# Kernel optimization log

Measured on AMD Instinct MI355X. Metric: run time of the kernel, lower is better.

## Reference

```python
import jax, jax.numpy as jnp
import numpy as np

HIDDEN = 1024
N_HEAD = 16
HEAD_DIM = HIDDEN // N_HEAD


def setup_inputs() -> dict:
    key = jax.random.key(0)
    k1, k2, k3 = jax.random.split(key, 3)
    B, S = 4, 2048
    x = jax.random.normal(k1, (B, S, HIDDEN), dtype=jnp.float32)
    # nn.Linear(hidden, 3*hidden, bias=False): weight [3*hidden, hidden]
    w_qkv = jax.random.normal(k2, (3 * HIDDEN, HIDDEN), dtype=jnp.float32) * (HIDDEN ** -0.5)
    w_out = jax.random.normal(k3, (HIDDEN, HIDDEN), dtype=jnp.float32) * (HIDDEN ** -0.5)
    return {"x": x, "w_qkv": w_qkv, "w_out": w_out}


def _rope(q, k):
    # q, k: [B, H, S, D]
    S, D = q.shape[-2], q.shape[-1]
    pos = jnp.arange(S, dtype=jnp.float32)[:, None]          # [S, 1]
    ids = jnp.arange(D // 2, dtype=jnp.float32)              # [D/2]
    theta = jnp.power(jnp.float32(10000.0), 2.0 * ids / D)   # [D/2]
    ang = pos / theta                                        # [S, D/2]
    # torch code: sin at even slots, cos at odd slots; then repeat_interleave(2)
    sin = jnp.repeat(jnp.sin(ang), 2, axis=-1)               # [S, D]
    cos = jnp.repeat(jnp.cos(ang), 2, axis=-1)               # [S, D]

    def rot(t):
        # stack([-t_odd, t_even], -1).reshape -> interleaved rotate-half
        t2 = jnp.stack([-t[..., 1::2], t[..., 0::2]], axis=-1).reshape(t.shape)
        return t * cos + t2 * sin

    return rot(q), rot(k)


def reference(x, w_qkv, w_out):
    B, S, _ = x.shape
    qkv = jnp.einsum('bsd,ed->bse', x, w_qkv)                # [B, S, 3*hidden]
    qkv = qkv.reshape(B, S, N_HEAD, 3 * HEAD_DIM).transpose(0, 2, 1, 3)  # [B,H,S,3D]
    q, k, v = jnp.split(qkv, 3, axis=-1)                     # each [B,H,S,D]
    q, k = _rope(q, k)
    # NOTE: original forward never applies self.scale, mask (eval), or dropout.
    scores = jnp.einsum('bhqd,bhkd->bhqk', q, k)             # [B,H,S,S]
    probs = jax.nn.softmax(scores, axis=-1)
    out = jnp.einsum('bhqk,bhkd->bhqd', probs, v)            # [B,H,S,D]
    out = out.transpose(0, 2, 1, 3).reshape(B, S, HIDDEN)
    return jnp.einsum('bsd,ed->bse', out, w_out)
```

## Files before the change

### kernel.cpp

```cpp
#include <hip/hip_runtime.h>
#include <stdint.h>
#include <math.h>

#define NHEAD 16
#define HDIM 64
#define BATCH 4
#define SEQ 2048
#define NROWS (BATCH*SEQ)
#define LOG2E 1.4426950408889634f

typedef _Float16 f16x8 __attribute__((ext_vector_type(8)));
typedef _Float16 f16x4 __attribute__((ext_vector_type(4)));
typedef __fp16 h16x2 __attribute__((ext_vector_type(2)));
typedef float f32x4 __attribute__((ext_vector_type(4)));
typedef float f32x16 __attribute__((ext_vector_type(16)));
typedef unsigned int u32x4 __attribute__((ext_vector_type(4)));

typedef const __attribute__((address_space(1))) unsigned int* gas_ptr;
typedef __attribute__((address_space(3))) unsigned int* las_ptr;

__device__ __forceinline__ void gload_lds16(const void* g, void* l) {
  __builtin_amdgcn_global_load_lds((gas_ptr)g, (las_ptr)l, 16, 0, 0);
}

__device__ __forceinline__ float exp2_fast(float x) {
  float r; asm("v_exp_f32 %0, %1" : "=v"(r) : "v"(x)); return r;
}

__device__ __forceinline__ float max3f(float a, float b, float c) {
  float r; asm("v_max3_f32 %0, %1, %2, %3" : "=v"(r) : "v"(a), "v"(b), "v"(c)); return r;
}

__device__ __forceinline__ unsigned pku(float a, float b) {
  h16x2 p = __builtin_amdgcn_cvt_pkrtz(a, b);
  return __builtin_bit_cast(unsigned, p);
}

__device__ __forceinline__ float xhalf_max(float a) {
  float b;
  asm volatile("v_mov_b32 %0, %1" : "=v"(b) : "v"(a));
  asm volatile("v_permlane32_swap_b32 %0, %1" : "+v"(a), "+v"(b));
  return fmaxf(a, b);
}

__global__ void prep_kernel(const float* __restrict__ x,
                            const float* __restrict__ wq,
                            const float* __restrict__ wo,
                            unsigned short* __restrict__ xb,
                            unsigned short* __restrict__ wqb,
                            unsigned short* __restrict__ wob,
                            float2* __restrict__ tab) {
  const int idx = blockIdx.x * blockDim.x + threadIdx.x;
  const int stride = gridDim.x * blockDim.x;
  const int NS = SEQ * 32;
  const int N1 = NROWS * 1024 / 4;
  const int N2 = 3072 * 1024 / 4;
  const int N3 = 1024 * 1024 / 4;

  if (idx < NS) {
    int s = idx >> 5, j = idx & 31;
    float theta = powf(10000.0f, (float)j / 32.0f);
    float ang = (float)s / theta;
    tab[idx] = make_float2(sinf(ang), cosf(ang));
  }
  for (int i = idx; i < N1 + N2 + N3; i += stride) {
    const float* src; unsigned short* dst; int k;
    if (i < N1)            { src = x;  dst = xb;  k = i; }
    else if (i < N1 + N2)  { src = wq; dst = wqb; k = i - N1; }
    else                   { src = wo; dst = wob; k = i - N1 - N2; }
    float4 v = ((const float4*)src)[k];
    f16x4 h;
    h[0] = (_Float16)v.x; h[1] = (_Float16)v.y;
    h[2] = (_Float16)v.z; h[3] = (_Float16)v.w;
    ((f16x4*)dst)[k] = h;
  }
}

__global__ __launch_bounds__(256)
void gemm_qkv_f16(const unsigned short* __restrict__ A,
                  const unsigned short* __restrict__ B,
                  const float2* __restrict__ tab,
                  unsigned short* __restrict__ Qh,
                  unsigned short* __restrict__ Kh,
                  unsigned short* __restrict__ Vt) {
  const int K = 1024, nk = K >> 6;
  __shared__ unsigned short sA[2][128 * 64];
  __shared__ unsigned short sB[2][128 * 64];
  const int tid = threadIdx.x;
  const int lane = tid & 63;
  const int wave = tid >> 6;
  const int wr = wave >> 1, wc = wave & 1;
  const long m0 = (long)blockIdx.x * 128;
  const long n0 = (long)blockIdx.y * 128;

  f32x16 acc[2][2] = {};

  auto stage = [&](int buf, int kt) {
    const long k0 = (long)kt * 64;
    const char* Ab = (const char*)A;
    const char* Bb = (const char*)B;
#pragma unroll
    for (int qd = 0; qd < 4; ++qd) {
      int o = qd * 4096 + tid * 16;
      int row = o >> 7;
      int colb = (((o >> 4) & 7) ^ (row & 7)) << 4;
      gload_lds16(Ab + ((m0 + row) * K + k0) * 2 + colb, (char*)&sA[buf][0] + o);
      gload_lds16(Bb + ((n0 + row) * K + k0) * 2 + colb, (char*)&sB[buf][0] + o);
    }
  };

  const int q32 = lane & 31, hi = lane >> 5, r7 = q32 & 7;
  int offA[2][4], offB[2][4];
#pragma unroll
  for (int t = 0; t < 2; ++t)
#pragma unroll
    for (int s = 0; s < 4; ++s) {
      offA[t][s] = (wr * 64 + t * 32 + q32) * 64 + (((s * 2 + hi) ^ r7) << 3);
      offB[t][s] = (wc * 64 + t * 32 + q32) * 64 + (((s * 2 + hi) ^ r7) << 3);
    }

  stage(0, 0);
  __syncthreads();
  int cur = 0;

  for (int kt = 0; kt < nk; ++kt) {
    if (kt + 1 < nk) stage(cur ^ 1, kt + 1);
#pragma unroll
    for (int s = 0; s < 4; ++s) {
      f16x8 a0 = *(const f16x8*)&sA[cur][offA[0][s]];
      f16x8 a1 = *(const f16x8*)&sA[cur][offA[1][s]];
      f16x8 b0 = *(const f16x8*)&sB[cur][offB[0][s]];
      f16x8 b1 = *(const f16x8*)&sB[cur][offB[1][s]];
      acc[0][0] = __builtin_amdgcn_mfma_f32_32x32x16_f16(a0, b0, acc[0][0], 0, 0, 0);
      acc[0][1] = __builtin_amdgcn_mfma_f32_32x32x16_f16(a0, b1, acc[0][1], 0, 0, 0);
      acc[1][0] = __builtin_amdgcn_mfma_f32_32x32x16_f16(a1, b0, acc[1][0], 0, 0, 0);
      acc[1][1] = __builtin_amdgcn_mfma_f32_32x32x16_f16(a1, b1, acc[1][1], 0, 0, 0);
    }
    __syncthreads();
    cur ^= 1;
  }

  const int rb0 = (int)m0 + wr * 64;
  const int bidx = rb0 >> 11;
  const int s0 = rb0 & 2047;
#pragma unroll
  for (int tn = 0; tn < 2; ++tn) {
    const int cbase = (int)n0 + wc * 64 + tn * 32;
    const int hh = cbase / 192;
    const int offc = cbase - hh * 192;
    const int part = offc >> 6;
    const int d = (offc & 63) + q32;
    const long bh_ = (long)(bidx * 16 + hh);
    if (part < 2) {
      _Float16* dst = (_Float16*)(part == 0 ? Qh : Kh) + bh_ * SEQ * 64 + d;
      const float qs = (part == 0) ? LOG2E : 1.0f;
      const float2* tp = tab + (d >> 1);
      const int sgn = q32 & 1;
#pragma unroll
      for (int tm = 0; tm < 2; ++tm)
#pragma unroll
        for (int rg = 0; rg < 16; ++rg) {
          int s = s0 + tm * 32 + (rg & 3) + 8 * (rg >> 2) + 4 * hi;
          float v = acc[tm][tn][rg];
          float p = __shfl_xor(v, 1, 64);
          float2 sc = tp[(long)s * 32];
          float rot = sgn ? (v * sc.y + p * sc.x) : (v * sc.y - p * sc.x);
          dst[(long)s * 64] = (_Float16)(rot * qs);
        }
    } else {
      _Float16* dst = (_Float16*)Vt + (bh_ * 64 + d) * SEQ;
#pragma unroll
      for (int tm = 0; tm < 2; ++tm)
#pragma unroll
        for (int rg = 0; rg < 16; ++rg) {
          int s = s0 + tm * 32 + (rg & 3) + 8 * (rg >> 2) + 4 * hi;
          dst[s] = (_Float16)acc[tm][tn][rg];
        }
    }
  }
}

__global__ __launch_bounds__(512, 4)
void attn_kernel(const unsigned short* __restrict__ Qh,
                 const unsigned short* __restrict__ Kh,
                 const unsigned short* __restrict__ Vt,
                 unsigned short* __restrict__ AOut) {
  __shared__ unsigned short sK[4][64 * 64];
  __shared__ unsigned short sV[4][64 * 64];

  const int NT = SEQ / 64;
  const int tid = threadIdx.x;
  const int w = tid >> 6, lane = tid & 63;
  const int q32 = lane & 31, hi = lane >> 5;

  const int bid = blockIdx.x;
  const int xcd = bid & 7, rest = bid >> 3;
  const int bh = (rest >> 3) * 8 + xcd;
  const int qt = rest & 7;
  const int b = bh >> 4, h = bh & 15;
  const int q = qt * 256 + w * 32 + q32;

  f16x8 aq[4];
#pragma unroll
  for (int ds = 0; ds < 4; ++ds)
    aq[ds] = *(const f16x8*)&Qh[((long)bh * SEQ + q) * 64 + ds * 16 + hi * 8];

  f32x16 acc0 = {}, acc1 = {}, accl = {};
  float mrow = -INFINITY;

  const int r7 = q32 & 7;
  int off[2][4];
#pragma unroll
  for (int t = 0; t < 2; ++t)
#pragma unroll
    for (int s = 0; s < 4; ++s)
      off[t][s] = (t * 32 + q32) * 64 + (((s * 2 + hi) ^ r7) << 3);

  const int cr = tid >> 3, cp = tid & 7, cps = cp ^ (cr & 7);
  const long kSrc0 = ((long)bh * SEQ + cr) * 64 + cps * 8;
  const long vSrc0 = ((long)bh * 64 + cr) * SEQ + cps * 8;

  auto stage = [&](int buf, int kt) {
    gload_lds16(&Kh[kSrc0 + (long)kt * 4096], (char*)&sK[buf][0] + tid * 16);
    gload_lds16(&Vt[vSrc0 + (long)kt * 64],   (char*)&sV[buf][0] + tid * 16);
  };

  f16x8 vones;
#pragma unroll
  for (int j = 0; j < 8; ++j) vones[j] = (_Float16)1.0f;

#define MKPA(dst, S, R0) {                                        \
    unsigned A0 = pku(S[R0 + 0], S[R0 + 1]);                      \
    unsigned A1 = pku(S[R0 + 2], S[R0 + 3]);                      \
    unsigned B0 = pku(S[R0 + 4], S[R0 + 5]);                      \
    unsigned B1 = pku(S[R0 + 6], S[R0 + 7]);                      \
    asm("v_permlane32_swap_b32 %0, %1" : "+v"(A0), "+v"(B0));     \
    asm("v_permlane32_swap_b32 %0, %1" : "+v"(A1), "+v"(B1));     \
    u32x4 tt; tt[0] = A0; tt[1] = A1; tt[2] = B0; tt[3] = B1;     \
    dst = __builtin_bit_cast(f16x8, tt); }

  auto tile = [&](int t) {
    const unsigned short* Kb = &sK[t & 3][0];
    const unsigned short* Vb = &sV[t & 3][0];

    f32x16 s0v = {}, s1v = {};
    __builtin_amdgcn_s_setprio(1);
#pragma unroll
    for (int ds = 0; ds < 4; ++ds) {
      f16x8 k0 = *(const f16x8*)&Kb[off[0][ds]];
      f16x8 k1 = *(const f16x8*)&Kb[off[1][ds]];
      s0v = __builtin_amdgcn_mfma_f32_32x32x16_f16(k0, aq[ds], s0v, 0, 0, 0);
      s1v = __builtin_amdgcn_mfma_f32_32x32x16_f16(k1, aq[ds], s1v, 0, 0, 0);
    }
    __builtin_amdgcn_s_setprio(0);

    float t0 = max3f(s0v[0], s0v[1], s0v[2]);
    float t1 = max3f(s0v[3], s0v[4], s0v[5]);
    float t2 = max3f(s0v[6], s0v[7], s0v[8]);
    float t3 = max3f(s0v[9], s0v[10], s0v[11]);
    float t4 = max3f(s0v[12], s0v[13], s0v[14]);
    float t5 = max3f(s0v[15], s1v[0], s1v[1]);
    float t6 = max3f(s1v[2], s1v[3], s1v[4]);
    float t7 = max3f(s1v[5], s1v[6], s1v[7]);
    float t8 = max3f(s1v[8], s1v[9], s1v[10]);
    float t9 = max3f(s1v[11], s1v[12], s1v[13]);
    float t10 = fmaxf(s1v[14], s1v[15]);
    float u0 = max3f(t0, t1, t2);
    float u1 = max3f(t3, t4, t5);
    float u2 = max3f(t6, t7, t8);
    float u3 = fmaxf(t9, t10);
    float tmax = xhalf_max(fmaxf(max3f(u0, u1, u2), u3));

    if (__any(tmax > mrow + 8.0f)) {
      float mnew = fmaxf(mrow, tmax);
      float al = exp2_fast(mrow - mnew);
      mrow = mnew;
#pragma unroll
      for (int r = 0; r < 16; ++r) { acc0[r] *= al; acc1[r] *= al; accl[r] *= al; }
    }
    const float mr = mrow;

#pragma unroll
    for (int r = 0; r < 16; ++r) {
      s0v[r] = exp2_fast(s0v[r] - mr);
      s1v[r] = exp2_fast(s1v[r] - mr);
    }

    f16x8 pa[4];
    MKPA(pa[0], s0v, 0);
    MKPA(pa[1], s0v, 8);
    MKPA(pa[2], s1v, 0);
    MKPA(pa[3], s1v, 8);

    __builtin_amdgcn_s_setprio(1);
#pragma unroll
    for (int ks = 0; ks < 4; ++ks) {
      f16x8 v0 = *(const f16x8*)&Vb[off[0][ks]];
      f16x8 v1 = *(const f16x8*)&Vb[off[1][ks]];
      acc0 = __builtin_amdgcn_mfma_f32_32x32x16_f16(v0, pa[ks], acc0, 0, 0, 0);
      acc1 = __builtin_amdgcn_mfma_f32_32x32x16_f16(v1, pa[ks], acc1, 0, 0, 0);
      accl = __builtin_amdgcn_mfma_f32_32x32x16_f16(vones, pa[ks], accl, 0, 0, 0);
    }
    __builtin_amdgcn_s_setprio(0);
  };

  stage(0, 0); stage(1, 1);
  __syncthreads();

  for (int it = 0; it < NT / 2; ++it) {
    const int t0 = it * 2;
    if (it + 1 < NT / 2) { stage((t0 + 2) & 3, t0 + 2); stage((t0 + 3) & 3, t0 + 3); }
    tile(t0);
    tile(t0 + 1);
    __syncthreads();
  }

  float inv = 1.f / accl[0];
  const long obase = ((long)b * SEQ + q) * 1024 + h * 64;
#define EPI(ACCV, DT)                                              \
  {                                                                \
    _Pragma("unroll")                                              \
    for (int rg = 0; rg < 4; ++rg) {                               \
      f16x4 o;                                                     \
      _Pragma("unroll")                                            \
      for (int e = 0; e < 4; ++e)                                  \
        o[e] = (_Float16)(ACCV[rg * 4 + e] * inv);                 \
      *(f16x4*)&AOut[obase + DT * 32 + rg * 8 + hi * 4] = o;       \
    }                                                              \
  }
  EPI(acc0, 0);
  EPI(acc1, 1);
}

__global__ __launch_bounds__(256)
void gemm_out_f16(const unsigned short* __restrict__ A,
                  const unsigned short* __restrict__ B,
                  float* __restrict__ C, int M, int N, int K) {
  __shared__ unsigned short sA[2][128 * 64];
  __shared__ unsigned short sB[2][128 * 64];
  const int tid = threadIdx.x;
  const int lane = tid & 63;
  const int wave = tid >> 6;
  const int wr = wave >> 1, wc = wave & 1;
  const long m0 = (long)blockIdx.x * 128;
  const long n0 = (long)blockIdx.y * 128;

  f32x16 acc[2][2] = {};

  auto stage = [&](int buf, int kt) {
    const long k0 = (long)kt * 64;
    const char* Ab = (const char*)A;
    const char* Bb = (const char*)B;
#pragma unroll
    for (int qd = 0; qd < 4; ++qd) {
      int o = qd * 4096 + tid * 16;
      int row = o >> 7;
      int colb = (((o >> 4) & 7) ^ (row & 7)) << 4;
      gload_lds16(Ab + ((m0 + row) * K + k0) * 2 + colb, (char*)&sA[buf][0] + o);
      gload_lds16(Bb + ((n0 + row) * K + k0) * 2 + colb, (char*)&sB[buf][0] + o);
    }
  };

  const int q32 = lane & 31, hi = lane >> 5, r7 = q32 & 7;
  int offA[2][4], offB[2][4];
#pragma unroll
  for (int t = 0; t < 2; ++t)
#pragma unroll
    for (int s = 0; s < 4; ++s) {
      offA[t][s] = (wr * 64 + t * 32 + q32) * 64 + (((s * 2 + hi) ^ r7) << 3);
      offB[t][s] = (wc * 64 + t * 32 + q32) * 64 + (((s * 2 + hi) ^ r7) << 3);
    }

  const int nk = K >> 6;
  stage(0, 0);
  __syncthreads();
  int cur = 0;

  for (int kt = 0; kt < nk; ++kt) {
    if (kt + 1 < nk) stage(cur ^ 1, kt + 1);
#pragma unroll
    for (int s = 0; s < 4; ++s) {
      f16x8 a0 = *(const f16x8*)&sA[cur][offA[0][s]];
      f16x8 a1 = *(const f16x8*)&sA[cur][offA[1][s]];
      f16x8 b0 = *(const f16x8*)&sB[cur][offB[0][s]];
      f16x8 b1 = *(const f16x8*)&sB[cur][offB[1][s]];
      acc[0][0] = __builtin_amdgcn_mfma_f32_32x32x16_f16(a0, b0, acc[0][0], 0, 0, 0);
      acc[0][1] = __builtin_amdgcn_mfma_f32_32x32x16_f16(a0, b1, acc[0][1], 0, 0, 0);
      acc[1][0] = __builtin_amdgcn_mfma_f32_32x32x16_f16(a1, b0, acc[1][0], 0, 0, 0);
      acc[1][1] = __builtin_amdgcn_mfma_f32_32x32x16_f16(a1, b1, acc[1][1], 0, 0, 0);
    }
    __syncthreads();
    cur ^= 1;
  }

  const long rbase = m0 + wr * 64;
#pragma unroll
  for (int tn = 0; tn < 2; ++tn) {
    const long col = n0 + wc * 64 + tn * 32 + q32;
#pragma unroll
    for (int tm = 0; tm < 2; ++tm)
#pragma unroll
      for (int rg = 0; rg < 16; ++rg) {
        long row = rbase + tm * 32 + (rg & 3) + 8 * (rg >> 2) + 4 * hi;
        C[row * N + col] = acc[tm][tn][rg];
      }
  }
}

extern "C" void kernel_launch(void* const* d_in, const int* in_sizes, int n_in,
                              void* d_out, int out_size, void* d_ws, size_t ws_size,
                              hipStream_t stream) {
  const float* x     = (const float*)d_in[0];
  const float* w_qkv = (const float*)d_in[1];
  const float* w_out = (const float*)d_in[2];
  float* out = (float*)d_out;
  char* ws = (char*)d_ws;

  unsigned short* xb    = (unsigned short*)(ws + 0);
  unsigned short* attnb = xb;
  unsigned short* wqkvb = (unsigned short*)(ws + 16777216);
  unsigned short* woutb = (unsigned short*)(ws + 23068672);
  unsigned short* Qh    = (unsigned short*)(ws + 25165824);
  unsigned short* Kh    = (unsigned short*)(ws + 41943040);
  unsigned short* Vt    = (unsigned short*)(ws + 58720256);
  float2*         tab   = (float2*)(ws + 75497472);

  prep_kernel<<<2048, 256, 0, stream>>>(x, w_qkv, w_out, xb, wqkvb, woutb, tab);
  gemm_qkv_f16<<<dim3(64, 24), 256, 0, stream>>>(xb, wqkvb, tab, Qh, Kh, Vt);
  attn_kernel<<<512, 512, 0, stream>>>(Qh, Kh, Vt, attnb);
  gemm_out_f16<<<dim3(64, 8), 256, 0, stream>>>(attnb, woutb, out, NROWS, 1024, 1024);
}
```

Before: 200.6 us.

## Triple-buffer GEMM k-loop with 32-wide K tiles and explicit vmcnt waits

Both projection GEMMs move from double-buffered 64-wide K tiles to a three-stage ring of 32-wide K tiles. Loads run two stages ahead, with explicit s_waitcnt vmcnt and a bare barrier replacing __syncthreads. Each stage's LDS fragments are read before the next prefetch is issued. The LDS layout is repacked (two rows per 128-byte line with a new swizzle) and launch bounds request 3 blocks per CU. The aim is better overlap of global loads with MFMA and higher occupancy, at the cost of twice as many barriers and more complex index math.

Measured after the change: 205.0 us. +2.2%, slower.

```diff
diff --git a/kernel.cpp b/kernel.cpp
--- a/kernel.cpp
+++ b/kernel.cpp
@@ -76,16 +76,16 @@
   }
 }
 
-__global__ __launch_bounds__(256)
+__global__ __launch_bounds__(256, 3)
 void gemm_qkv_f16(const unsigned short* __restrict__ A,
                   const unsigned short* __restrict__ B,
                   const float2* __restrict__ tab,
                   unsigned short* __restrict__ Qh,
                   unsigned short* __restrict__ Kh,
                   unsigned short* __restrict__ Vt) {
-  const int K = 1024, nk = K >> 6;
-  __shared__ unsigned short sA[2][128 * 64];
-  __shared__ unsigned short sB[2][128 * 64];
+  const int K = 1024, nk = K >> 5;
+  __shared__ unsigned short sA[3][64 * 64];
+  __shared__ unsigned short sB[3][64 * 64];
   const int tid = threadIdx.x;
   const int lane = tid & 63;
   const int wave = tid >> 6;
@@ -95,49 +95,72 @@
 
   f32x16 acc[2][2] = {};
 
+  int gg[2], kc[2];
+#pragma unroll
+  for (int l = 0; l < 2; ++l) {
+    int o = l * 4096 + tid * 16;
+    int lr = o >> 7;
+    int qp = ((o >> 4) & 7) ^ (lr & 7);
+    gg[l] = 2 * lr + (qp >> 2);
+    kc[l] = qp & 3;
+  }
+
   auto stage = [&](int buf, int kt) {
-    const long k0 = (long)kt * 64;
     const char* Ab = (const char*)A;
     const char* Bb = (const char*)B;
 #pragma unroll
-    for (int qd = 0; qd < 4; ++qd) {
-      int o = qd * 4096 + tid * 16;
-      int row = o >> 7;
-      int colb = (((o >> 4) & 7) ^ (row & 7)) << 4;
-      gload_lds16(Ab + ((m0 + row) * K + k0) * 2 + colb, (char*)&sA[buf][0] + o);
-      gload_lds16(Bb + ((n0 + row) * K + k0) * 2 + colb, (char*)&sB[buf][0] + o);
+    for (int l = 0; l < 2; ++l) {
+      long ka = (long)kt * 32 + kc[l] * 8;
+      int dst = l * 4096 + tid * 16;
+      gload_lds16(Ab + ((m0 + gg[l]) * K + ka) * 2, (char*)&sA[buf][0] + dst);
+      gload_lds16(Bb + ((n0 + gg[l]) * K + ka) * 2, (char*)&sB[buf][0] + dst);
     }
   };
 
-  const int q32 = lane & 31, hi = lane >> 5, r7 = q32 & 7;
-  int offA[2][4], offB[2][4];
-#pragma unroll
-  for (int t = 0; t < 2; ++t)
-#pragma unroll
-    for (int s = 0; s < 4; ++s) {
-      offA[t][s] = (wr * 64 + t * 32 + q32) * 64 + (((s * 2 + hi) ^ r7) << 3);
-      offB[t][s] = (wc * 64 + t * 32 + q32) * 64 + (((s * 2 + hi) ^ r7) << 3);
-    }
-
-  stage(0, 0);
-  __syncthreads();
-  int cur = 0;
+  const int q32 = lane & 31, hi = lane >> 5;
+  const int rsw = (q32 >> 1) & 7;
+  int offA[2][2], offB[2][2];
+#pragma unroll
+  for (int tm = 0; tm < 2; ++tm)
+#pragma unroll
+    for (int s = 0; s < 2; ++s) {
+      int ch = ((q32 & 1) << 2) + s * 2 + hi;
+      int lrA = wr * 32 + tm * 16 + (q32 >> 1);
+      int lrB = wc * 32 + tm * 16 + (q32 >> 1);
+      offA[tm][s] = lrA * 64 + ((ch ^ rsw) << 3);
+      offB[tm][s] = lrB * 64 + ((ch ^ rsw) << 3);
+    }
+
+  stage(0, 0); stage(1, 1);
+  asm volatile("s_waitcnt vmcnt(4)" ::: "memory");
+  __builtin_amdgcn_s_barrier();
+  __builtin_amdgcn_sched_barrier(0);
 
   for (int kt = 0; kt < nk; ++kt) {
-    if (kt + 1 < nk) stage(cur ^ 1, kt + 1);
-#pragma unroll
-    for (int s = 0; s < 4; ++s) {
-      f16x8 a0 = *(const f16x8*)&sA[cur][offA[0][s]];
-      f16x8 a1 = *(const f16x8*)&sA[cur][offA[1][s]];
-      f16x8 b0 = *(const f16x8*)&sB[cur][offB[0][s]];
-      f16x8 b1 = *(const f16x8*)&sB[cur][offB[1][s]];
-      acc[0][0] = __builtin_amdgcn_mfma_f32_32x32x16_f16(a0, b0, acc[0][0], 0, 0, 0);
-      acc[0][1] = __builtin_amdgcn_mfma_f32_32x32x16_f16(a0, b1, acc[0][1], 0, 0, 0);
-      acc[1][0] = __builtin_amdgcn_mfma_f32_32x32x16_f16(a1, b0, acc[1][0], 0, 0, 0);
-      acc[1][1] = __builtin_amdgcn_mfma_f32_32x32x16_f16(a1, b1, acc[1][1], 0, 0, 0);
-    }
-    __syncthreads();
-    cur ^= 1;
+    const int cb = kt % 3;
+    f16x8 a0s0 = *(const f16x8*)&sA[cb][offA[0][0]];
+    f16x8 a1s0 = *(const f16x8*)&sA[cb][offA[1][0]];
+    f16x8 b0s0 = *(const f16x8*)&sB[cb][offB[0][0]];
+    f16x8 b1s0 = *(const f16x8*)&sB[cb][offB[1][0]];
+    f16x8 a0s1 = *(const f16x8*)&sA[cb][offA[0][1]];
+    f16x8 a1s1 = *(const f16x8*)&sA[cb][offA[1][1]];
+    f16x8 b0s1 = *(const f16x8*)&sB[cb][offB[0][1]];
+    f16x8 b1s1 = *(const f16x8*)&sB[cb][offB[1][1]];
+    if (kt + 2 < nk) stage((kt + 2) % 3, kt + 2);
+    acc[0][0] = __builtin_amdgcn_mfma_f32_32x32x16_f16(a0s0, b0s0, acc[0][0], 0, 0, 0);
+    acc[0][1] = __builtin_amdgcn_mfma_f32_32x32x16_f16(a0s0, b1s0, acc[0][1], 0, 0, 0);
+    acc[1][0] = __builtin_amdgcn_mfma_f32_32x32x16_f16(a1s0, b0s0, acc[1][0], 0, 0, 0);
+    acc[1][1] = __builtin_amdgcn_mfma_f32_32x32x16_f16(a1s0, b1s0, acc[1][1], 0, 0, 0);
+    acc[0][0] = __builtin_amdgcn_mfma_f32_32x32x16_f16(a0s1, b0s1, acc[0][0], 0, 0, 0);
+    acc[0][1] = __builtin_amdgcn_mfma_f32_32x32x16_f16(a0s1, b1s1, acc[0][1], 0, 0, 0);
+    acc[1][0] = __builtin_amdgcn_mfma_f32_32x32x16_f16(a1s1, b0s1, acc[1][0], 0, 0, 0);
+    acc[1][1] = __builtin_amdgcn_mfma_f32_32x32x16_f16(a1s1, b1s1, acc[1][1], 0, 0, 0);
+    if (kt + 1 < nk) {
+      if (kt + 2 < nk) asm volatile("s_waitcnt vmcnt(4)" ::: "memory");
+      else             asm volatile("s_waitcnt vmcnt(0)" ::: "memory");
+      __builtin_amdgcn_s_barrier();
+      __builtin_amdgcn_sched_barrier(0);
+    }
   }
 
   const int rb0 = (int)m0 + wr * 64;
@@ -332,12 +355,13 @@
   EPI(acc1, 1);
 }
 
-__global__ __launch_bounds__(256)
+__global__ __launch_bounds__(256, 3)
 void gemm_out_f16(const unsigned short* __restrict__ A,
                   const unsigned short* __restrict__ B,
                   float* __restrict__ C, int M, int N, int K) {
-  __shared__ unsigned short sA[2][128 * 64];
-  __shared__ unsigned short sB[2][128 * 64];
+  const int nk = K >> 5;
+  __shared__ unsigned short sA[3][64 * 64];
+  __shared__ unsigned short sB[3][64 * 64];
   const int tid = threadIdx.x;
   const int lane = tid & 63;
   const int wave = tid >> 6;
@@ -347,50 +371,72 @@
 
   f32x16 acc[2][2] = {};
 
+  int gg[2], kc[2];
+#pragma unroll
+  for (int l = 0; l < 2; ++l) {
+    int o = l * 4096 + tid * 16;
+    int lr = o >> 7;
+    int qp = ((o >> 4) & 7) ^ (lr & 7);
+    gg[l] = 2 * lr + (qp >> 2);
+    kc[l] = qp & 3;
+  }
+
   auto stage = [&](int buf, int kt) {
-    const long k0 = (long)kt * 64;
     const char* Ab = (const char*)A;
     const char* Bb = (const char*)B;
 #pragma unroll
-    for (int qd = 0; qd < 4; ++qd) {
-      int o = qd * 4096 + tid * 16;
-      int row = o >> 7;
-      int colb = (((o >> 4) & 7) ^ (row & 7)) << 4;
-      gload_lds16(Ab + ((m0 + row) * K + k0) * 2 + colb, (char*)&sA[buf][0] + o);
-      gload_lds16(Bb + ((n0 + row) * K + k0) * 2 + colb, (char*)&sB[buf][0] + o);
+    for (int l = 0; l < 2; ++l) {
+      long ka = (long)kt * 32 + kc[l] * 8;
+      int dst = l * 4096 + tid * 16;
+      gload_lds16(Ab + ((m0 + gg[l]) * K + ka) * 2, (char*)&sA[buf][0] + dst);
+      gload_lds16(Bb + ((n0 + gg[l]) * K + ka) * 2, (char*)&sB[buf][0] + dst);
     }
   };
 
-  const int q32 = lane & 31, hi = lane >> 5, r7 = q32 & 7;
-  int offA[2][4], offB[2][4];
-#pragma unroll
-  for (int t = 0; t < 2; ++t)
-#pragma unroll
-    for (int s = 0; s < 4; ++s) {
-      offA[t][s] = (wr * 64 + t * 32 + q32) * 64 + (((s * 2 + hi) ^ r7) << 3);
-      offB[t][s] = (wc * 64 + t * 32 + q32) * 64 + (((s * 2 + hi) ^ r7) << 3);
-    }
-
-  const int nk = K >> 6;
-  stage(0, 0);
-  __syncthreads();
-  int cur = 0;
+  const int q32 = lane & 31, hi = lane >> 5;
+  const int rsw = (q32 >> 1) & 7;
+  int offA[2][2], offB[2][2];
+#pragma unroll
+  for (int tm = 0; tm < 2; ++tm)
+#pragma unroll
+    for (int s = 0; s < 2; ++s) {
+      int ch = ((q32 & 1) << 2) + s * 2 + hi;
+      int lrA = wr * 32 + tm * 16 + (q32 >> 1);
+      int lrB = wc * 32 + tm * 16 + (q32 >> 1);
+      offA[tm][s] = lrA * 64 + ((ch ^ rsw) << 3);
+      offB[tm][s] = lrB * 64 + ((ch ^ rsw) << 3);
+    }
+
+  stage(0, 0); stage(1, 1);
+  asm volatile("s_waitcnt vmcnt(4)" ::: "memory");
+  __builtin_amdgcn_s_barrier();
+  __builtin_amdgcn_sched_barrier(0);
 
   for (int kt = 0; kt < nk; ++kt) {
-    if (kt + 1 < nk) stage(cur ^ 1, kt + 1);
-#pragma unroll
-    for (int s = 0; s < 4; ++s) {
-      f16x8 a0 = *(const f16x8*)&sA[cur][offA[0][s]];
-      f16x8 a1 = *(const f16x8*)&sA[cur][offA[1][s]];
-      f16x8 b0 = *(const f16x8*)&sB[cur][offB[0][s]];
-      f16x8 b1 = *(const f16x8*)&sB[cur][offB[1][s]];
-      acc[0][0] = __builtin_amdgcn_mfma_f32_32x32x16_f16(a0, b0, acc[0][0], 0, 0, 0);
-      acc[0][1] = __builtin_amdgcn_mfma_f32_32x32x16_f16(a0, b1, acc[0][1], 0, 0, 0);
-      acc[1][0] = __builtin_amdgcn_mfma_f32_32x32x16_f16(a1, b0, acc[1][0], 0, 0, 0);
-      acc[1][1] = __builtin_amdgcn_mfma_f32_32x32x16_f16(a1, b1, acc[1][1], 0, 0, 0);
-    }
-    __syncthreads();
-    cur ^= 1;
+    const int cb = kt % 3;
+    f16x8 a0s0 = *(const f16x8*)&sA[cb][offA[0][0]];
+    f16x8 a1s0 = *(const f16x8*)&sA[cb][offA[1][0]];
+    f16x8 b0s0 = *(const f16x8*)&sB[cb][offB[0][0]];
+    f16x8 b1s0 = *(const f16x8*)&sB[cb][offB[1][0]];
+    f16x8 a0s1 = *(const f16x8*)&sA[cb][offA[0][1]];
+    f16x8 a1s1 = *(const f16x8*)&sA[cb][offA[1][1]];
+    f16x8 b0s1 = *(const f16x8*)&sB[cb][offB[0][1]];
+    f16x8 b1s1 = *(const f16x8*)&sB[cb][offB[1][1]];
+    if (kt + 2 < nk) stage((kt + 2) % 3, kt + 2);
+    acc[0][0] = __builtin_amdgcn_mfma_f32_32x32x16_f16(a0s0, b0s0, acc[0][0], 0, 0, 0);
+    acc[0][1] = __builtin_amdgcn_mfma_f32_32x32x16_f16(a0s0, b1s0, acc[0][1], 0, 0, 0);
+    acc[1][0] = __builtin_amdgcn_mfma_f32_32x32x16_f16(a1s0, b0s0, acc[1][0], 0, 0, 0);
+    acc[1][1] = __builtin_amdgcn_mfma_f32_32x32x16_f16(a1s0, b1s0, acc[1][1], 0, 0, 0);
+    acc[0][0] = __builtin_amdgcn_mfma_f32_32x32x16_f16(a0s1, b0s1, acc[0][0], 0, 0, 0);
+    acc[0][1] = __builtin_amdgcn_mfma_f32_32x32x16_f16(a0s1, b1s1, acc[0][1], 0, 0, 0);
+    acc[1][0] = __builtin_amdgcn_mfma_f32_32x32x16_f16(a1s1, b0s1, acc[1][0], 0, 0, 0);
+    acc[1][1] = __builtin_amdgcn_mfma_f32_32x32x16_f16(a1s1, b1s1, acc[1][1], 0, 0, 0);
+    if (kt + 1 < nk) {
+      if (kt + 2 < nk) asm volatile("s_waitcnt vmcnt(4)" ::: "memory");
+      else             asm volatile("s_waitcnt vmcnt(0)" ::: "memory");
+      __builtin_amdgcn_s_barrier();
+      __builtin_amdgcn_sched_barrier(0);
+    }
   }
 
   const long rbase = m0 + wr * 64;
```
